# Optimization experiments

Hardware: AMD Instinct MI355X
Metric: run time of the kernel (lower is better)

The kernel has to match this reference:

```python
import jax, jax.numpy as jnp
import numpy as np

N_E = 1024
E_DIM = 512
LEGACY_CLUSTER = 0.2
LEGACY_ENERGY = 0.2


def setup_inputs() -> dict:
    key = jax.random.key(0)
    k1, k2 = jax.random.split(key)
    B, T = 64, 512
    key_soft = jax.random.normal(k1, (B, T, E_DIM), dtype=jnp.float32)
    zero_ts_mask = jnp.zeros((B,), dtype=bool)
    # nn.Embedding(1+n_e, e_dim) initialized uniform(-1/n_e, 1/n_e)
    emb_weight = jax.random.uniform(k2, (N_E + 1, E_DIM), dtype=jnp.float32,
                                    minval=-1.0 / N_E, maxval=1.0 / N_E)
    return {"key_soft": key_soft, "zero_ts_mask": zero_ts_mask, "emb_weight": emb_weight}


def _compute_indices(d3, zero_ts_mask, n_e):
    # d3: [B, T, n_e+1] squared distances (treated as constants: torch.no_grad)
    ind0 = jnp.clip(jnp.argmin(d3[:, 0, :], axis=1), 0, n_e - 1)
    ind0 = jnp.where(zero_ts_mask, 0, ind0)

    def step(ind, d_t):
        # d_t: [B, n_e+1]; neighbor-constrained argmin: stay at ind or move to ind+1
        d_here = jnp.take_along_axis(d_t, ind[:, None], axis=1)[:, 0]
        ind_next = jnp.clip(ind + 1, 0, n_e - 1)
        d_next = jnp.take_along_axis(d_t, ind_next[:, None], axis=1)[:, 0]
        new_ind = jnp.where(d_here <= d_next, ind, ind_next)
        return new_ind, new_ind

    d_rest = jnp.swapaxes(d3[:, 1:, :], 0, 1)  # [T-1, B, n_e+1] time-major
    _, inds_rest = jax.lax.scan(step, ind0, d_rest)
    return jnp.concatenate([ind0[:, None], jnp.swapaxes(inds_rest, 0, 1)], axis=1)  # [B, T]


def reference(key_soft, zero_ts_mask, emb_weight):
    sg = jax.lax.stop_gradient
    B, T, e_dim = key_soft.shape
    n_e = emb_weight.shape[0] - 1
    ksf = key_soft.reshape(-1, e_dim)  # [B*T, e_dim]
    # squared euclidean distances to all 1+n_e codes: [B*T, n_e+1]
    d = (jnp.sum(ksf ** 2, axis=1, keepdims=True)
         + jnp.sum(emb_weight ** 2, axis=1)
         - 2.0 * jnp.einsum('bd,nd->bn', ksf, emb_weight))
    min_indices = jnp.argmin(d, axis=1)  # [B*T]
    d3 = d.reshape(B, T, n_e + 1)
    encoding_indices = _compute_indices(sg(d3), zero_ts_mask, n_e)  # [B, T]

    key_hard_here = emb_weight[encoding_indices]        # [B, T, e_dim]
    key_hard_next = emb_weight[encoding_indices + 1]    # [B, T, e_dim]
    key_min = emb_weight[min_indices].reshape(B, T, e_dim)

    key_em_here = (jnp.sum((sg(key_soft) - key_hard_here) ** 2, axis=-1)
                   + jnp.sum((key_soft - sg(key_hard_here)) ** 2, axis=-1) * LEGACY_ENERGY)
    key_em_next = (jnp.sum((sg(key_soft) - key_hard_next) ** 2, axis=-1)
                   + jnp.sum((key_soft - sg(key_hard_next)) ** 2, axis=-1) * LEGACY_ENERGY)
    key_energy_mat = key_em_next - key_em_here  # [B, T]

    ind_change = (encoding_indices[:, 1:] - encoding_indices[:, :-1]).astype(bool)
    key_energy_change = (key_energy_mat[:, 1:] - key_energy_mat[:, :-1]) * jnp.where(ind_change, 0.0, 1.0)
    eps = 1e-06 / n_e
    loss_key_energy_descent = jnp.maximum(key_energy_change + eps, 0.0).mean()

    loss_min_indices = (jnp.sum((sg(key_soft) - key_min) ** 2, axis=-1)
                        + jnp.sum((key_soft - sg(key_min)) ** 2, axis=-1) * LEGACY_CLUSTER)
    reg_persist_mat = jnp.exp(-key_em_next)
    e_normal_mat = jnp.where(key_em_here > loss_min_indices - eps,
                             key_em_here - loss_min_indices + eps,
                             key_em_here) + reg_persist_mat
    e_abnormal_mat = key_em_next + jnp.exp(-key_em_here)

    key_hard = key_soft + sg(key_hard_here - key_soft)  # straight-through
    v = jnp.max(jnp.max(encoding_indices, axis=1) - jnp.min(encoding_indices, axis=1))
    return (key_hard, encoding_indices, v, loss_key_energy_descent,
            key_energy_mat, e_normal_mat, e_abnormal_mat)
```

## Files before the change

### kernel.cpp

```cpp
#include <hip/hip_runtime.h>
#include <math.h>

typedef unsigned char u8;
typedef unsigned short u16;
typedef unsigned int u32;
typedef __attribute__((ext_vector_type(8))) short bf16x8;
typedef __attribute__((ext_vector_type(4))) float f32x4;

#define O1 16777216
#define O2 16809984
#define O3 16809985
#define O4 16809986
#define O5 16842754
#define O6 16875522

#define W_COLSQ 0
#define W_MINV  4352
#define W_MINI  2101504
#define W_SF    4198656
#define W_SL    6426880
#define W_BITS  8524032
#define W_MIDX  12718336
#define W_ENC   12849408
#define W_V     12980480

__device__ __forceinline__ u16 f2bf(float x) {
  u32 u = __float_as_uint(x);
  u32 r = u + 0x7FFFu + ((u >> 16) & 1u);
  return (u16)(r >> 16);
}
__device__ __forceinline__ float bf2f(u16 h) { return __uint_as_float((u32)h << 16); }

__global__ __launch_bounds__(256) void k0_colsq(const float* __restrict__ emb,
                                                float* __restrict__ colsq) {
  int w = threadIdx.x >> 6, lane = threadIdx.x & 63;
  int c = blockIdx.x * 4 + w;
  if (c >= 1025) return;
  const float4* e4 = (const float4*)(emb + (size_t)c * 512);
  float4 a = e4[lane * 2], b = e4[lane * 2 + 1];
  float p = a.x * a.x + a.y * a.y + a.z * a.z + a.w * a.w
          + b.x * b.x + b.y * b.y + b.z * b.z + b.w * b.w;
  #pragma unroll
  for (int off = 32; off; off >>= 1) p += __shfl_xor(p, off);
  if (lane == 0) colsq[c] = p;
}

__global__ __launch_bounds__(256) void k1_gemm(const float* __restrict__ ksf,
                                               const float* __restrict__ emb,
                                               const float* __restrict__ colsq,
                                               float* __restrict__ minv, int* __restrict__ mini,
                                               float* __restrict__ sF, float* __restrict__ sL,
                                               u8* __restrict__ bits) {
  __shared__ float smemf[8448];
  char* smc = (char*)smemf;
  const int tid = threadIdx.x, bid = blockIdx.x;
  const int g = bid >> 6;
  const int cbk = (bid >> 3) & 7;
  const int rb = g * 8 + (bid & 7);
  const int r0 = rb * 128, c0 = cbk * 128;
  const int lane = tid & 63, w = tid >> 6;
  const int wr = w >> 1, wc = w & 1;
  const int q = lane >> 4, li = lane & 15;

  int offS[4], baseA[4], baseB[4];
  #pragma unroll
  for (int i = 0; i < 4; i++) {
    int p = tid + (i << 8);
    int row = p >> 3, q8 = p & 7;
    offS[i] = row * 64 + ((q8 * 8) ^ (((row >> 1) & 3) << 4));
    baseA[i] = (r0 + row) * 128 + q8;
    baseB[i] = (c0 + row) * 128 + q8;
  }
  int foA[4], foB[4];
  #pragma unroll
  for (int m = 0; m < 4; m++) {
    int row = wr * 64 + m * 16 + li;
    foA[m] = row * 64 + ((q * 16) ^ (((row >> 1) & 3) << 4));
    int col = wc * 64 + m * 16 + li;
    foB[m] = col * 64 + ((q * 16) ^ (((col >> 1) & 3) << 4));
  }

  f32x4 acc[4][4];
  #pragma unroll
  for (int m = 0; m < 4; m++)
    #pragma unroll
    for (int n = 0; n < 4; n++) acc[m][n] = (f32x4){0.f, 0.f, 0.f, 0.f};

  const float4* A4 = (const float4*)ksf;
  const float4* B4 = (const float4*)emb;
  float4 ra[4], rbv[4];
  #pragma unroll
  for (int i = 0; i < 4; i++) { ra[i] = A4[baseA[i]]; rbv[i] = B4[baseB[i]]; }

  for (int kt = 0; kt < 16; kt++) {
    __syncthreads();
    #pragma unroll
    for (int i = 0; i < 4; i++) {
      float4 v = ra[i];
      ushort4 h, l;
      h.x = f2bf(v.x); l.x = f2bf(v.x - bf2f(h.x));
      h.y = f2bf(v.y); l.y = f2bf(v.y - bf2f(h.y));
      h.z = f2bf(v.z); l.z = f2bf(v.z - bf2f(h.z));
      h.w = f2bf(v.w); l.w = f2bf(v.w - bf2f(h.w));
      *(ushort4*)(smc + offS[i]) = h;
      *(ushort4*)(smc + 8192 + offS[i]) = l;
      float4 u = rbv[i];
      ushort4 hb, lb;
      hb.x = f2bf(u.x); lb.x = f2bf(u.x - bf2f(hb.x));
      hb.y = f2bf(u.y); lb.y = f2bf(u.y - bf2f(hb.y));
      hb.z = f2bf(u.z); lb.z = f2bf(u.z - bf2f(hb.z));
      hb.w = f2bf(u.w); lb.w = f2bf(u.w - bf2f(hb.w));
      *(ushort4*)(smc + 16384 + offS[i]) = hb;
      *(ushort4*)(smc + 24576 + offS[i]) = lb;
    }
    if (kt < 15) {
      #pragma unroll
      for (int i = 0; i < 4; i++) {
        ra[i] = A4[baseA[i] + (kt + 1) * 8];
        rbv[i] = B4[baseB[i] + (kt + 1) * 8];
      }
    }
    __syncthreads();
    bf16x8 fA[4], fB[4], fX[4];
    #pragma unroll
    for (int m = 0; m < 4; m++) fA[m] = *(const bf16x8*)(smc + foA[m]);
    #pragma unroll
    for (int n = 0; n < 4; n++) fB[n] = *(const bf16x8*)(smc + 16384 + foB[n]);
    #pragma unroll
    for (int m = 0; m < 4; m++)
      #pragma unroll
      for (int n = 0; n < 4; n++)
        acc[m][n] = __builtin_amdgcn_mfma_f32_16x16x32_bf16(fA[m], fB[n], acc[m][n], 0, 0, 0);
    #pragma unroll
    for (int n = 0; n < 4; n++) fX[n] = *(const bf16x8*)(smc + 24576 + foB[n]);
    #pragma unroll
    for (int m = 0; m < 4; m++)
      #pragma unroll
      for (int n = 0; n < 4; n++)
        acc[m][n] = __builtin_amdgcn_mfma_f32_16x16x32_bf16(fA[m], fX[n], acc[m][n], 0, 0, 0);
    #pragma unroll
    for (int m = 0; m < 4; m++) fA[m] = *(const bf16x8*)(smc + 8192 + foA[m]);
    #pragma unroll
    for (int m = 0; m < 4; m++)
      #pragma unroll
      for (int n = 0; n < 4; n++)
        acc[m][n] = __builtin_amdgcn_mfma_f32_16x16x32_bf16(fA[m], fB[n], acc[m][n], 0, 0, 0);
  }

  float cs4[4];
  #pragma unroll
  for (int n = 0; n < 4; n++) cs4[n] = colsq[c0 + wc * 64 + n * 16 + li];
  const int ct = tid & 15, rt = tid >> 4;
  for (int h = 0; h < 2; h++) {
    __syncthreads();
    if (wr == h) {
      #pragma unroll
      for (int m = 0; m < 4; m++) {
        int rl = m * 16 + q * 4;
        #pragma unroll
        for (int n = 0; n < 4; n++) {
          int cl = wc * 64 + n * 16 + li;
          #pragma unroll
          for (int r = 0; r < 4; r++)
            smemf[(rl + r) * 132 + cl] = fmaf(acc[m][n][r], -2.0f, cs4[n]);
        }
      }
    }
    __syncthreads();
    #pragma unroll
    for (int j = 0; j < 4; j++) {
      int rl = rt * 4 + j;
      int rowg = r0 + h * 64 + rl;
      const float* sp = &smemf[rl * 132 + ct * 8];
      float4 sa = *(const float4*)sp, sb = *(const float4*)(sp + 4);
      float s[8] = {sa.x, sa.y, sa.z, sa.w, sb.x, sb.y, sb.z, sb.w};
      float sn0 = __shfl_down(s[0], 1, 16);
      u32 bv = 0;
      #pragma unroll
      for (int i = 0; i < 7; i++) bv |= (s[i] <= s[i + 1]) ? (1u << i) : 0u;
      bv |= (s[7] <= sn0) ? 0x80u : 0u;
      bits[rowg * 128 + cbk * 16 + ct] = (u8)bv;
      int cbase = c0 + ct * 8;
      float mv = s[0]; int mi = cbase;
      #pragma unroll
      for (int i = 1; i < 8; i++) if (s[i] < mv) { mv = s[i]; mi = cbase + i; }
      #pragma unroll
      for (int d = 4; d >= 1; d >>= 1) {
        float ov = __shfl_xor(mv, d, 8);
        int oi = __shfl_xor(mi, d, 8);
        if (ov < mv || (ov == mv && oi < mi)) { mv = ov; mi = oi; }
      }
      int sb64 = cbk * 2 + (ct >> 3);
      if ((ct & 7) == 0) {
        minv[rowg * 16 + sb64] = mv;
        mini[rowg * 16 + sb64] = mi;
        sF[rowg * 17 + sb64] = s[0];
      }
      if ((ct & 7) == 7) sL[rowg * 16 + sb64] = s[7];
    }
  }
}

__global__ __launch_bounds__(256) void k1b_col1024(const float* __restrict__ ksf,
                                                   const float* __restrict__ emb,
                                                   const float* __restrict__ colsq,
                                                   float* __restrict__ sF) {
  int wid = threadIdx.x >> 6, lane = threadIdx.x & 63;
  int row = blockIdx.x * 4 + wid;
  const float4* ks4 = (const float4*)(ksf + (size_t)row * 512);
  const float4* e4 = (const float4*)(emb + (size_t)1024 * 512);
  float4 a = ks4[lane * 2], b = ks4[lane * 2 + 1];
  float4 ea = e4[lane * 2], eb = e4[lane * 2 + 1];
  float p = a.x * ea.x + a.y * ea.y + a.z * ea.z + a.w * ea.w
          + b.x * eb.x + b.y * eb.y + b.z * eb.z + b.w * eb.w;
  #pragma unroll
  for (int off = 32; off; off >>= 1) p += __shfl_xor(p, off);
  if (lane == 0) sF[row * 17 + 16] = fmaf(p, -2.0f, colsq[1024]);
}

__global__ __launch_bounds__(256) void k2_combine(const float* __restrict__ minv,
                                                  const int* __restrict__ mini,
                                                  const float* __restrict__ sF,
                                                  const float* __restrict__ sL,
                                                  u8* __restrict__ bits,
                                                  int* __restrict__ midx, int* __restrict__ vslot) {
  int row = blockIdx.x * 256 + threadIdx.x;
  if (blockIdx.x == 0 && threadIdx.x == 0) *vslot = 0;
  float bv = minv[row * 16];
  int bi = mini[row * 16];
  #pragma unroll
  for (int cb = 1; cb < 16; cb++) {
    float v = minv[row * 16 + cb];
    int ii = mini[row * 16 + cb];
    if (v < bv) { bv = v; bi = ii; }
  }
  float s1024 = sF[row * 17 + 16];
  if (s1024 < bv) { bv = s1024; bi = 1024; }
  midx[row] = bi;
  #pragma unroll
  for (int cb = 0; cb < 16; cb++) {
    float nb = (cb < 15) ? sF[row * 17 + cb + 1] : s1024;
    u8 bit = (sL[row * 16 + cb] <= nb) ? (u8)0x80 : (u8)0;
    int a = row * 128 + cb * 8 + 7;
    bits[a] = (u8)((bits[a] & 0x7F) | bit);
  }
}

__global__ __launch_bounds__(256) void k3_scan(const u8* __restrict__ bits,
                                               const int* __restrict__ midx,
                                               const u8* __restrict__ mask,
                                               int* __restrict__ enc, int* __restrict__ vslot) {
  __shared__ u32 bl[256 * 32];
  __shared__ int el[512];
  int b = blockIdx.x, tid = threadIdx.x;
  const u32* bw = (const u32*)bits;
  for (int phase = 0; phase < 2; phase++) {
    int t0 = 1 + phase * 256;
    int nt = phase ? 255 : 256;
    __syncthreads();
    for (int w = tid; w < nt * 32; w += 256)
      bl[w] = bw[(size_t)(b * 512 + t0) * 32 + w];
    __syncthreads();
    if (tid == 0) {
      int ind;
      if (phase == 0) {
        int mi = midx[b * 512];
        ind = mi < 1023 ? mi : 1023;
        if (mask[b]) ind = 0;
        el[0] = ind;
      } else ind = el[256];
      for (int tt = 0; tt < nt; tt++) {
        if (ind < 1023) {
          u32 w = bl[tt * 32 + (ind >> 5)];
          ind += 1 - (int)((w >> (ind & 31)) & 1u);
        }
        el[t0 + tt] = ind;
      }
    }
  }
  __syncthreads();
  for (int t = tid; t < 512; t += 256) enc[b * 512 + t] = el[t];
  if (tid == 0) atomicMax(vslot, el[511] - el[0]);
}

__global__ __launch_bounds__(256) void k4_energy(const float* __restrict__ ksf,
                                                 const float* __restrict__ emb,
                                                 const int* __restrict__ enc_a,
                                                 const int* __restrict__ midx,
                                                 float* __restrict__ out) {
  int wid = threadIdx.x >> 6, lane = threadIdx.x & 63;
  int row = blockIdx.x * 4 + wid;
  int eh = enc_a[row];
  int mi = midx[row];
  const float4* ks4 = (const float4*)(ksf + (size_t)row * 512);
  const float4* h4 = (const float4*)(emb + (size_t)eh * 512);
  const float4* n4 = (const float4*)(emb + (size_t)(eh + 1) * 512);
  const float4* m4 = (const float4*)(emb + (size_t)mi * 512);
  float ph = 0.f, pn = 0.f, pm = 0.f;
  float4 kh[2];
  #pragma unroll
  for (int u = 0; u < 2; u++) {
    float4 k = ks4[lane * 2 + u], h = h4[lane * 2 + u], n = n4[lane * 2 + u], m = m4[lane * 2 + u];
    float d;
    d = k.x - h.x; ph = fmaf(d, d, ph);
    d = k.y - h.y; ph = fmaf(d, d, ph);
    d = k.z - h.z; ph = fmaf(d, d, ph);
    d = k.w - h.w; ph = fmaf(d, d, ph);
    d = k.x - n.x; pn = fmaf(d, d, pn);
    d = k.y - n.y; pn = fmaf(d, d, pn);
    d = k.z - n.z; pn = fmaf(d, d, pn);
    d = k.w - n.w; pn = fmaf(d, d, pn);
    d = k.x - m.x; pm = fmaf(d, d, pm);
    d = k.y - m.y; pm = fmaf(d, d, pm);
    d = k.z - m.z; pm = fmaf(d, d, pm);
    d = k.w - m.w; pm = fmaf(d, d, pm);
    kh[u].x = k.x + (h.x - k.x);
    kh[u].y = k.y + (h.y - k.y);
    kh[u].z = k.z + (h.z - k.z);
    kh[u].w = k.w + (h.w - k.w);
  }
  #pragma unroll
  for (int off = 32; off; off >>= 1) {
    ph += __shfl_xor(ph, off);
    pn += __shfl_xor(pn, off);
    pm += __shfl_xor(pm, off);
  }
  float4* o0 = (float4*)out;
  o0[(size_t)row * 128 + lane * 2] = kh[0];
  o0[(size_t)row * 128 + lane * 2 + 1] = kh[1];
  if (lane == 0) {
    const float epsN = 9.765625e-10f;
    float kemh = ph + ph * 0.2f;
    float kemn = pn + pn * 0.2f;
    float lmin = pm + pm * 0.2f;
    float lminu = fminf(lmin, kemh);
    out[O1 + row] = (float)eh;
    out[O4 + row] = kemn - kemh;
    float env = (kemh > lminu - epsN) ? ((kemh - lminu) + epsN) : kemh;
    out[O5 + row] = env + expf(-kemn);
    out[O6 + row] = kemn + expf(-kemh);
  }
}

__global__ __launch_bounds__(1024) void k5_loss(const float* __restrict__ kem,
                                                const int* __restrict__ enc,
                                                const int* __restrict__ vslot,
                                                float* __restrict__ out) {
  __shared__ float red[1024];
  int tid = threadIdx.x;
  const float epsN = 9.765625e-10f;
  float p = 0.f;
  for (int i = tid; i < 64 * 511; i += 1024) {
    int b = i / 511, tt = i - b * 511;
    int row = b * 512 + tt + 1;
    float diff = kem[row] - kem[row - 1];
    if (enc[row] != enc[row - 1]) diff = 0.f;
    float v = diff + epsN;
    p += (v > 0.f) ? v : 0.f;
  }
  red[tid] = p;
  __syncthreads();
  for (int s = 512; s; s >>= 1) {
    if (tid < s) red[tid] += red[tid + s];
    __syncthreads();
  }
  if (tid == 0) {
    out[O3] = red[0] / 32704.0f;
    out[O2] = (float)(*vslot);
  }
}

extern "C" void kernel_launch(void* const* d_in, const int* in_sizes, int n_in,
                              void* d_out, int out_size, void* d_ws, size_t ws_size,
                              hipStream_t stream) {
  const float* ksf = (const float*)d_in[0];
  const u8* mask = (const u8*)d_in[1];
  const float* emb = (const float*)d_in[2];
  float* out = (float*)d_out;
  char* ws = (char*)d_ws;
  float* colsq = (float*)(ws + W_COLSQ);
  float* minv = (float*)(ws + W_MINV);
  int* mini = (int*)(ws + W_MINI);
  float* sF = (float*)(ws + W_SF);
  float* sL = (float*)(ws + W_SL);
  u8* bits = (u8*)(ws + W_BITS);
  int* midx = (int*)(ws + W_MIDX);
  int* enc = (int*)(ws + W_ENC);
  int* vslot = (int*)(ws + W_V);

  hipLaunchKernelGGL(k0_colsq, dim3(257), dim3(256), 0, stream, emb, colsq);
  hipLaunchKernelGGL(k1_gemm, dim3(2048), dim3(256), 0, stream, ksf, emb, colsq,
                     minv, mini, sF, sL, bits);
  hipLaunchKernelGGL(k1b_col1024, dim3(8192), dim3(256), 0, stream, ksf, emb, colsq, sF);
  hipLaunchKernelGGL(k2_combine, dim3(128), dim3(256), 0, stream, minv, mini, sF, sL,
                     bits, midx, vslot);
  hipLaunchKernelGGL(k3_scan, dim3(64), dim3(256), 0, stream, bits, midx, mask, enc, vslot);
  hipLaunchKernelGGL(k4_energy, dim3(8192), dim3(256), 0, stream, ksf, emb, enc, midx, out);
  hipLaunchKernelGGL(k5_loss, dim3(1), dim3(1024), 0, stream, out + O4, enc, vslot, out);
}
```

Before: 234.1 us.

## Precompute bf16 hi/lo codebook split once and stream it via global_load_lds

The codebook's bf16 hi/lo split is now computed once in the colsq kernel and written to workspace, so the GEMM no longer repeats that conversion in every block. The GEMM loads the pre-split B tiles straight into LDS with global_load_lds, using swizzled addresses. The A-side split switches to the packed v_cvt_pk_bf16_f32 instruction. In exchange, the prefetch of the next A tile moves after the second barrier, which may reduce overlap, and the workspace grows.

New measurement: 228.0 us. -2.6%, faster.

```diff
diff --git a/kernel.cpp b/kernel.cpp
--- a/kernel.cpp
+++ b/kernel.cpp
@@ -23,16 +23,26 @@
 #define W_MIDX  12718336
 #define W_ENC   12849408
 #define W_V     12980480
-
-__device__ __forceinline__ u16 f2bf(float x) {
-  u32 u = __float_as_uint(x);
-  u32 r = u + 0x7FFFu + ((u >> 16) & 1u);
-  return (u16)(r >> 16);
-}
-__device__ __forceinline__ float bf2f(u16 h) { return __uint_as_float((u32)h << 16); }
+#define W_EH    13000704
+#define W_EL    14050304
+
+__device__ __forceinline__ u32 cvt_pk(float lo, float hi) {
+  u32 r;
+  asm volatile("v_cvt_pk_bf16_f32 %0, %1, %2" : "=v"(r) : "v"(lo), "v"(hi));
+  return r;
+}
+__device__ __forceinline__ float asf(u32 u) { return __uint_as_float(u); }
+
+__device__ __forceinline__ void gload_lds16(const void* g, void* l) {
+  __builtin_amdgcn_global_load_lds(
+      (const __attribute__((address_space(1))) unsigned int*)g,
+      (__attribute__((address_space(3))) unsigned int*)l, 16, 0, 0);
+}
 
 __global__ __launch_bounds__(256) void k0_colsq(const float* __restrict__ emb,
-                                                float* __restrict__ colsq) {
+                                                float* __restrict__ colsq,
+                                                u32* __restrict__ emb_hi,
+                                                u32* __restrict__ emb_lo) {
   int w = threadIdx.x >> 6, lane = threadIdx.x & 63;
   int c = blockIdx.x * 4 + w;
   if (c >= 1025) return;
@@ -43,10 +53,22 @@
   #pragma unroll
   for (int off = 32; off; off >>= 1) p += __shfl_xor(p, off);
   if (lane == 0) colsq[c] = p;
+  u32 h0 = cvt_pk(a.x, a.y), h1 = cvt_pk(a.z, a.w);
+  u32 h2 = cvt_pk(b.x, b.y), h3 = cvt_pk(b.z, b.w);
+  float l0 = a.x - asf(h0 << 16), l1 = a.y - asf(h0 & 0xFFFF0000u);
+  float l2 = a.z - asf(h1 << 16), l3 = a.w - asf(h1 & 0xFFFF0000u);
+  float l4 = b.x - asf(h2 << 16), l5 = b.y - asf(h2 & 0xFFFF0000u);
+  float l6 = b.z - asf(h3 << 16), l7 = b.w - asf(h3 & 0xFFFF0000u);
+  uint4 hv; hv.x = h0; hv.y = h1; hv.z = h2; hv.w = h3;
+  uint4 lv; lv.x = cvt_pk(l0, l1); lv.y = cvt_pk(l2, l3);
+  lv.z = cvt_pk(l4, l5); lv.w = cvt_pk(l6, l7);
+  ((uint4*)emb_hi)[c * 64 + lane] = hv;
+  ((uint4*)emb_lo)[c * 64 + lane] = lv;
 }
 
 __global__ __launch_bounds__(256) void k1_gemm(const float* __restrict__ ksf,
-                                               const float* __restrict__ emb,
+                                               const u32* __restrict__ emb_hi,
+                                               const u32* __restrict__ emb_lo,
                                                const float* __restrict__ colsq,
                                                float* __restrict__ minv, int* __restrict__ mini,
                                                float* __restrict__ sF, float* __restrict__ sL,
@@ -62,15 +84,23 @@
   const int wr = w >> 1, wc = w & 1;
   const int q = lane >> 4, li = lane & 15;
 
-  int offS[4], baseA[4], baseB[4];
+  int offS[4], baseA[4];
   #pragma unroll
   for (int i = 0; i < 4; i++) {
     int p = tid + (i << 8);
     int row = p >> 3, q8 = p & 7;
     offS[i] = row * 64 + ((q8 * 8) ^ (((row >> 1) & 3) << 4));
     baseA[i] = (r0 + row) * 128 + q8;
-    baseB[i] = (c0 + row) * 128 + q8;
-  }
+  }
+  const int rowj0 = w * 32 + (lane >> 2), rowj1 = rowj0 + 16;
+  const int qb = lane & 3;
+  const int offB0 = (c0 + rowj0) * 1024 + ((qb ^ ((rowj0 >> 1) & 3)) << 4);
+  const int offB1 = (c0 + rowj1) * 1024 + ((qb ^ ((rowj1 >> 1) & 3)) << 4);
+  char* ldsB0 = smc + 16384 + w * 2048;
+  char* ldsB1 = ldsB0 + 1024;
+  const char* ebh = (const char*)emb_hi;
+  const char* ebl = (const char*)emb_lo;
+
   int foA[4], foB[4];
   #pragma unroll
   for (int m = 0; m < 4; m++) {
@@ -87,40 +117,38 @@
     for (int n = 0; n < 4; n++) acc[m][n] = (f32x4){0.f, 0.f, 0.f, 0.f};
 
   const float4* A4 = (const float4*)ksf;
-  const float4* B4 = (const float4*)emb;
-  float4 ra[4], rbv[4];
-  #pragma unroll
-  for (int i = 0; i < 4; i++) { ra[i] = A4[baseA[i]]; rbv[i] = B4[baseB[i]]; }
+  float4 ra[4];
+  #pragma unroll
+  for (int i = 0; i < 4; i++) ra[i] = A4[baseA[i]];
 
   for (int kt = 0; kt < 16; kt++) {
     __syncthreads();
+    {
+      int ko = kt * 64;
+      gload_lds16(ebh + offB0 + ko, ldsB0);
+      gload_lds16(ebh + offB1 + ko, ldsB1);
+      gload_lds16(ebl + offB0 + ko, ldsB0 + 8192);
+      gload_lds16(ebl + offB1 + ko, ldsB1 + 8192);
+    }
     #pragma unroll
     for (int i = 0; i < 4; i++) {
       float4 v = ra[i];
-      ushort4 h, l;
-      h.x = f2bf(v.x); l.x = f2bf(v.x - bf2f(h.x));
-      h.y = f2bf(v.y); l.y = f2bf(v.y - bf2f(h.y));
-      h.z = f2bf(v.z); l.z = f2bf(v.z - bf2f(h.z));
-      h.w = f2bf(v.w); l.w = f2bf(v.w - bf2f(h.w));
-      *(ushort4*)(smc + offS[i]) = h;
-      *(ushort4*)(smc + 8192 + offS[i]) = l;
-      float4 u = rbv[i];
-      ushort4 hb, lb;
-      hb.x = f2bf(u.x); lb.x = f2bf(u.x - bf2f(hb.x));
-      hb.y = f2bf(u.y); lb.y = f2bf(u.y - bf2f(hb.y));
-      hb.z = f2bf(u.z); lb.z = f2bf(u.z - bf2f(hb.z));
-      hb.w = f2bf(u.w); lb.w = f2bf(u.w - bf2f(hb.w));
-      *(ushort4*)(smc + 16384 + offS[i]) = hb;
-      *(ushort4*)(smc + 24576 + offS[i]) = lb;
-    }
+      u32 w0 = cvt_pk(v.x, v.y), w1 = cvt_pk(v.z, v.w);
+      float lx = v.x - asf(w0 << 16);
+      float ly = v.y - asf(w0 & 0xFFFF0000u);
+      float lz = v.z - asf(w1 << 16);
+      float lw = v.w - asf(w1 & 0xFFFF0000u);
+      u32 m0 = cvt_pk(lx, ly), m1 = cvt_pk(lz, lw);
+      uint2 hv; hv.x = w0; hv.y = w1;
+      uint2 lv; lv.x = m0; lv.y = m1;
+      *(uint2*)(smc + offS[i]) = hv;
+      *(uint2*)(smc + 8192 + offS[i]) = lv;
+    }
+    __syncthreads();
     if (kt < 15) {
       #pragma unroll
-      for (int i = 0; i < 4; i++) {
-        ra[i] = A4[baseA[i] + (kt + 1) * 8];
-        rbv[i] = B4[baseB[i] + (kt + 1) * 8];
-      }
-    }
-    __syncthreads();
+      for (int i = 0; i < 4; i++) ra[i] = A4[baseA[i] + (kt + 1) * 8];
+    }
     bf16x8 fA[4], fB[4], fX[4];
     #pragma unroll
     for (int m = 0; m < 4; m++) fA[m] = *(const bf16x8*)(smc + foA[m]);
@@ -387,9 +415,11 @@
   int* midx = (int*)(ws + W_MIDX);
   int* enc = (int*)(ws + W_ENC);
   int* vslot = (int*)(ws + W_V);
-
-  hipLaunchKernelGGL(k0_colsq, dim3(257), dim3(256), 0, stream, emb, colsq);
-  hipLaunchKernelGGL(k1_gemm, dim3(2048), dim3(256), 0, stream, ksf, emb, colsq,
+  u32* emb_hi = (u32*)(ws + W_EH);
+  u32* emb_lo = (u32*)(ws + W_EL);
+
+  hipLaunchKernelGGL(k0_colsq, dim3(257), dim3(256), 0, stream, emb, colsq, emb_hi, emb_lo);
+  hipLaunchKernelGGL(k1_gemm, dim3(2048), dim3(256), 0, stream, ksf, emb_hi, emb_lo, colsq,
                      minv, mini, sF, sL, bits);
   hipLaunchKernelGGL(k1b_col1024, dim3(8192), dim3(256), 0, stream, ksf, emb, colsq, sF);
   hipLaunchKernelGGL(k2_combine, dim3(128), dim3(256), 0, stream, minv, mini, sF, sL,
```
